# Optimization experiments

Hardware: AMD Instinct MI355X
Metric: run time of the kernel (lower is better)

Reference implementation:

```python
import jax, jax.numpy as jnp
import numpy as np

NUM_Q_HEADS = 16
NUM_KV_HEADS = 4
HEAD_DIM = 128
HIDDEN = NUM_Q_HEADS * HEAD_DIM
SCALE = 1.0 / HEAD_DIM ** 0.5
NUM_REP = NUM_Q_HEADS // NUM_KV_HEADS
S, B = 2048, 2


def setup_inputs() -> dict:
    key = jax.random.key(0)
    kq, kk, kv = jax.random.split(key, 3)
    query = jax.random.normal(kq, (S, B, NUM_Q_HEADS, HEAD_DIM), dtype=jnp.float32)
    k = jax.random.normal(kk, (S, B, NUM_KV_HEADS, HEAD_DIM), dtype=jnp.float32)
    v = jax.random.normal(kv, (S, B, NUM_KV_HEADS, HEAD_DIM), dtype=jnp.float32)
    return {"query": query, "key": k, "value": v}


def _attn(query, key, value):
    # GQA: repeat kv heads [S,B,Hkv,D] -> [S,B,Hq,D]
    key = jnp.repeat(key, NUM_REP, axis=2)
    value = jnp.repeat(value, NUM_REP, axis=2)
    # fp32 scores, causal mask, softmax (matches torch reference math)
    q32, k32, v32 = query.astype(jnp.float32), key.astype(jnp.float32), value.astype(jnp.float32)
    scores = jnp.einsum('sbhd,tbhd->bhst', q32, k32) * SCALE  # [B,Hq,S,S]
    s = scores.shape[-1]
    causal = jnp.tril(jnp.ones((s, s), dtype=bool))
    scores = jnp.where(causal, scores, -jnp.inf)
    attn = jax.nn.softmax(scores, axis=-1)
    out = jnp.einsum('bhst,tbhd->sbhd', attn, v32)  # [S,B,Hq,D]
    return out.astype(query.dtype).reshape(out.shape[0], out.shape[1], HIDDEN)


def reference(query, key, value) -> jnp.ndarray:
    return _attn(query, key, value)
```

## Files before the change

kernel.cpp:

```cpp
#include <hip/hip_runtime.h>
#include <cstdint>
#include <cstddef>

#define S_LEN 2048
#define BATCH 2
#define HQ    16
#define HKV   4
#define DH    128
#define KVB   64
#define QT0   64
#define KVB0  32
#define VP    40
#define PP    40

typedef float  f4     __attribute__((ext_vector_type(4)));
typedef float  f32x4  __attribute__((ext_vector_type(4)));
typedef float  f32x16 __attribute__((ext_vector_type(16)));
typedef short  short8 __attribute__((ext_vector_type(8)));
typedef unsigned u32x4 __attribute__((ext_vector_type(4)));
typedef __bf16 bf16x8 __attribute__((ext_vector_type(8)));

__device__ __forceinline__ unsigned short f2bf(float x) {
    unsigned u = __builtin_bit_cast(unsigned, x);
    u += 0x7fffu + ((u >> 16) & 1u);
    return (unsigned short)(u >> 16);
}
__device__ __forceinline__ void gld16(const void* g, void* l) {
    __builtin_amdgcn_global_load_lds(
        (const __attribute__((address_space(1))) unsigned int*)g,
        (__attribute__((address_space(3))) unsigned int*)l, 16, 0, 0);
}
__device__ __forceinline__ unsigned cvtpk_bf16(float lo, float hi) {
    unsigned r;
    asm("v_cvt_pk_bf16_f32 %0, %1, %2" : "=v"(r) : "v"(lo), "v"(hi));
    return r;
}

__global__ __launch_bounds__(256)
void prep_k(const float* __restrict__ K, short* __restrict__ out) {
    const int blk = blockIdx.x, bh = blk >> 5, tile = blk & 31, tid = threadIdx.x;
    const int r  = tid >> 2;
    const int s  = tile * 64 + r;
    const int c0 = (tid & 3) * 32;
    const float* src = K + ((size_t)s * (BATCH * HKV) + bh) * DH + c0;
    short* dst = out + ((size_t)bh * S_LEN + s) * DH;
    const int sw = (r & 7) << 3;
    #pragma unroll
    for (int ks = 0; ks < 4; ++ks) {
        f4 a  = ((const f4*)src)[ks * 2];
        f4 b2 = ((const f4*)src)[ks * 2 + 1];
        short8 o;
        #pragma unroll
        for (int j = 0; j < 4; ++j) { o[j] = (short)f2bf(a[j]); o[4 + j] = (short)f2bf(b2[j]); }
        *(short8*)&dst[(c0 + ks * 8) ^ sw] = o;
    }
}

__global__ __launch_bounds__(256)
void prep_v(const float* __restrict__ V, short* __restrict__ out) {
    __shared__ short t[64][136];
    const int blk = blockIdx.x, bh = blk >> 5, tile = blk & 31, tid = threadIdx.x;
    {
        const int r  = tid >> 2;
        const int c0 = (tid & 3) * 32;
        const float* src = V + ((size_t)(tile * 64 + r) * (BATCH * HKV) + bh) * DH + c0;
        #pragma unroll
        for (int m = 0; m < 8; ++m) {
            f4 x = ((const f4*)src)[m];
            #pragma unroll
            for (int j = 0; j < 4; ++j) t[r][c0 + m * 4 + j] = (short)f2bf(x[j]);
        }
    }
    __syncthreads();
    {
        const int d   = tid >> 1;
        const int cc0 = (tid & 1) * 32;
        const int sw  = (d & 7) << 3;
        short* dst = out + (size_t)bh * (S_LEN * DH) + (size_t)tile * (64 * DH) + d * 64 + cc0;
        #pragma unroll
        for (int c8 = 0; c8 < 4; ++c8) {
            const int base = (cc0 + c8 * 8) ^ sw;
            short8 v;
            #pragma unroll
            for (int j = 0; j < 8; ++j) v[j] = t[base + j][d];
            ((short8*)dst)[c8] = v;
        }
    }
}

__global__ __launch_bounds__(512, 2)
void fattn_main(const float* __restrict__ Q, const short* __restrict__ Kb,
                const short* __restrict__ Vb, float* __restrict__ O)
{
    __shared__ short kbufs[2][KVB * DH];
    __shared__ short vbufs[2][DH * KVB];
    __shared__ float xbuf[8][32];

    const int bh  = blockIdx.y;
    const int b   = bh >> 4, h = bh & 15, hkv = h >> 2;
    const int bh2 = b * HKV + hkv;
    const int px  = blockIdx.x;
    const int tid = threadIdx.x;
    const int wid = tid >> 6;
    const int lane = tid & 63;
    const int lq  = lane & 31;
    const int hi  = lane >> 5;

    const int qx   = (wid < 4) ? (15 - px) : px;
    const int wq0  = qx * 128 + (wid & 3) * 32;
    const int tmask = wq0 >> 6;
    const int ntiles = 2 * (15 - px) + 2;

    const float QS = 0.127517244f;
    bf16x8 qf[8];
    {
        const float* qp = Q + ((size_t)(wq0 + lq) * BATCH + b) * (HQ * DH) + h * DH + 8 * hi;
        #pragma unroll
        for (int dstp = 0; dstp < 8; ++dstp) {
            f4 v0 = ((const f4*)(qp + dstp * 16))[0];
            f4 v1 = ((const f4*)(qp + dstp * 16))[1];
            short8 tq;
            #pragma unroll
            for (int j = 0; j < 4; ++j) {
                tq[j]     = (short)f2bf(v0[j] * QS);
                tq[4 + j] = (short)f2bf(v1[j] * QS);
            }
            qf[dstp] = __builtin_bit_cast(bf16x8, tq);
        }
    }

    f32x16 accO[4];
    #pragma unroll
    for (int dblk = 0; dblk < 4; ++dblk)
        #pragma unroll
        for (int r = 0; r < 16; ++r) accO[dblk][r] = 0.f;
    float m = -3.0e38f, dsum = 0.f;

    const char* ksrc = (const char*)(Kb + (size_t)bh2 * S_LEN * DH);
    const char* vsrc = (const char*)(Vb + (size_t)bh2 * S_LEN * DH);

    auto stage = [&](int t, int bufi) {
        const char* src = (wid < 4 ? ksrc : vsrc) + (size_t)t * 16384 + (size_t)(wid & 3) * 4096;
        char* dst = (char*)(wid < 4 ? &kbufs[bufi][0] : &vbufs[bufi][0]) + (wid & 3) * 4096;
        #pragma unroll
        for (int i = 0; i < 4; ++i) gld16(src + i * 1024 + lane * 16, dst + i * 1024);
    };

    stage(0, 0);
    __syncthreads();

    for (int t = 0; t < ntiles; ++t) {
        const int cur = t & 1;
        if (t + 1 < ntiles) stage(t + 1, cur ^ 1);
        if (t <= tmask) {
            const short* kc = kbufs[cur];
            const short* vc = vbufs[cur];

            f32x16 s0, s1;
            #pragma unroll
            for (int r = 0; r < 16; ++r) { s0[r] = 0.f; s1[r] = 0.f; }
            const int ksw = (lq & 7) << 3;
            const int kr0 = lq * DH, kr1 = (32 + lq) * DH;
            __builtin_amdgcn_s_setprio(1);
            #pragma unroll
            for (int dstp = 0; dstp < 8; ++dstp) {
                const int off = (dstp * 16 + 8 * hi) ^ ksw;
                short8 k0 = *(const short8*)&kc[kr0 + off];
                short8 k1 = *(const short8*)&kc[kr1 + off];
                s0 = __builtin_amdgcn_mfma_f32_32x32x16_bf16(
                    __builtin_bit_cast(bf16x8, k0), qf[dstp], s0, 0, 0, 0);
                s1 = __builtin_amdgcn_mfma_f32_32x32x16_bf16(
                    __builtin_bit_cast(bf16x8, k1), qf[dstp], s1, 0, 0, 0);
            }
            __builtin_amdgcn_s_setprio(0);

            if (t == tmask) {
                const int q = wq0 + lq;
                const int kvb = t * 64 + 4 * hi;
                #pragma unroll
                for (int r = 0; r < 16; ++r) {
                    const int crow = (r & 3) + 8 * (r >> 2);
                    if (kvb + crow > q)      s0[r] = -3.0e38f;
                    if (kvb + 32 + crow > q) s1[r] = -3.0e38f;
                }
            }

            float pm = fmaxf(s0[0], s1[0]);
            #pragma unroll
            for (int r = 1; r < 16; ++r) pm = fmaxf(pm, fmaxf(s0[r], s1[r]));
            pm = fmaxf(pm, __shfl_xor(pm, 32));

            if (!__all(pm <= m + 8.0f)) {
                const float mn = fmaxf(m, pm);
                const float al = __builtin_amdgcn_exp2f(m - mn);
                m = mn;
                if (lane < 32) xbuf[wid][lq] = al;
                #pragma unroll
                for (int g = 0; g < 4; ++g) {
                    f4 av = *(const f4*)&xbuf[wid][g * 8 + 4 * hi];
                    #pragma unroll
                    for (int i2 = 0; i2 < 4; ++i2) {
                        #pragma unroll
                        for (int dblk = 0; dblk < 4; ++dblk)
                            accO[dblk][g * 4 + i2] *= av[i2];
                    }
                }
                dsum *= al;
            }

            float rs = 0.f;
            #pragma unroll
            for (int r = 0; r < 16; ++r) { s0[r] = __builtin_amdgcn_exp2f(s0[r] - m); rs += s0[r]; }
            #pragma unroll
            for (int r = 0; r < 16; ++r) { s1[r] = __builtin_amdgcn_exp2f(s1[r] - m); rs += s1[r]; }
            rs += __shfl_xor(rs, 32);
            dsum += rs;

            bf16x8 pf[4];
            #pragma unroll
            for (int kst = 0; kst < 4; ++kst) {
                const int bo = (kst & 1) * 8;
                float p0, p1, p2, p3, p4, p5, p6, p7;
                if (kst < 2) {
                    p0 = s0[bo + 0]; p1 = s0[bo + 1]; p2 = s0[bo + 2]; p3 = s0[bo + 3];
                    p4 = s0[bo + 4]; p5 = s0[bo + 5]; p6 = s0[bo + 6]; p7 = s0[bo + 7];
                } else {
                    p0 = s1[bo + 0]; p1 = s1[bo + 1]; p2 = s1[bo + 2]; p3 = s1[bo + 3];
                    p4 = s1[bo + 4]; p5 = s1[bo + 5]; p6 = s1[bo + 6]; p7 = s1[bo + 7];
                }
                const unsigned c0 = cvtpk_bf16(p0, p1);
                const unsigned c1 = cvtpk_bf16(p2, p3);
                const unsigned c2 = cvtpk_bf16(p4, p5);
                const unsigned c3 = cvtpk_bf16(p6, p7);
                const unsigned sc0 = (unsigned)__shfl_xor((int)c0, 32);
                const unsigned sc1 = (unsigned)__shfl_xor((int)c1, 32);
                const unsigned sc2 = (unsigned)__shfl_xor((int)c2, 32);
                const unsigned sc3 = (unsigned)__shfl_xor((int)c3, 32);
                u32x4 pw;
                pw[0] = hi ? sc2 : c0;
                pw[1] = hi ? sc3 : c1;
                pw[2] = hi ? c2  : sc0;
                pw[3] = hi ? c3  : sc1;
                pf[kst] = __builtin_bit_cast(bf16x8, pw);
            }

            const int vsw = (lq & 7) << 3;
            __builtin_amdgcn_s_setprio(1);
            #pragma unroll
            for (int kst = 0; kst < 4; ++kst) {
                const int voff = kst * 16 + 8 * hi;
                #pragma unroll
                for (int dblk = 0; dblk < 4; ++dblk) {
                    const int d = dblk * 32 + lq;
                    short8 vv = *(const short8*)&vc[d * KVB + ((voff) ^ vsw)];
                    accO[dblk] = __builtin_amdgcn_mfma_f32_32x32x16_bf16(
                        pf[kst], __builtin_bit_cast(bf16x8, vv), accO[dblk], 0, 0, 0);
                }
            }
            __builtin_amdgcn_s_setprio(0);
        }
        __syncthreads();
    }

    if (lane < 32) xbuf[wid][lq] = dsum;
    #pragma unroll
    for (int g = 0; g < 4; ++g) {
        f4 dv = *(const f4*)&xbuf[wid][g * 8 + 4 * hi];
        #pragma unroll
        for (int i2 = 0; i2 < 4; ++i2) {
            const float inv = 1.0f / dv[i2];
            const int row = wq0 + g * 8 + i2 + 4 * hi;
            float* op = O + ((size_t)row * BATCH + b) * (HQ * DH) + h * DH + lq;
            #pragma unroll
            for (int dblk = 0; dblk < 4; ++dblk)
                op[dblk * 32] = accO[dblk][g * 4 + i2] * inv;
        }
    }
}

__global__ __launch_bounds__(256)
void fattn_fallback(const float* __restrict__ Q, const float* __restrict__ K,
                    const float* __restrict__ V, float* __restrict__ O)
{
    __shared__ short kbuf[KVB0 * DH];
    __shared__ short vbuf[DH * VP];
    __shared__ short pbuf[4][16 * PP];

    const int bh  = blockIdx.y;
    const int b   = bh >> 4, h = bh & 15, hkv = h >> 2;
    const int q0  = blockIdx.x * QT0;
    const int tid = threadIdx.x;
    const int wid = tid >> 6;
    const int lane = tid & 63;
    const int lr  = lane & 15;
    const int kb  = lane >> 4;
    const int qr  = q0 + wid * 16;

    const float QS = 0.127517244f;
    bf16x8 qf[4];
    {
        const float* qp = Q + ((size_t)(qr + lr) * BATCH + b) * (HQ * DH) + h * DH + kb * 8;
        #pragma unroll
        for (int ks = 0; ks < 4; ++ks) {
            f4 v0 = ((const f4*)(qp + ks * 32))[0];
            f4 v1 = ((const f4*)(qp + ks * 32))[1];
            short8 tq;
            #pragma unroll
            for (int j = 0; j < 4; ++j) {
                tq[j]     = (short)f2bf(v0[j] * QS);
                tq[4 + j] = (short)f2bf(v1[j] * QS);
            }
            qf[ks] = __builtin_bit_cast(bf16x8, tq);
        }
    }

    float mr[4], ls[4];
    f32x4 accO[8];
    #pragma unroll
    for (int r = 0; r < 4; ++r) { mr[r] = -3.0e38f; ls[r] = 0.0f; }
    #pragma unroll
    for (int d = 0; d < 8; ++d) accO[d] = (f32x4){0.f, 0.f, 0.f, 0.f};

    const int sr  = tid >> 3, sc = tid & 7;
    const int vr2 = (tid >> 4) * 2, vc8 = tid & 15;
    const int ntiles = q0 / KVB0 + 2;

    for (int t = 0; t < ntiles; ++t) {
        const int kv0 = t * KVB0;
        {
            const float* kp = K + ((size_t)(kv0 + sr) * BATCH + b) * (HKV * DH) + hkv * DH + sc * 16;
            f4 a0 = ((const f4*)kp)[0];
            f4 a1 = ((const f4*)kp)[1];
            f4 a2 = ((const f4*)kp)[2];
            f4 a3 = ((const f4*)kp)[3];
            short8 s0v, s1v;
            #pragma unroll
            for (int j = 0; j < 4; ++j) {
                s0v[j] = (short)f2bf(a0[j]); s0v[4 + j] = (short)f2bf(a1[j]);
                s1v[j] = (short)f2bf(a2[j]); s1v[4 + j] = (short)f2bf(a3[j]);
            }
            const int sw = (sr & 7) << 3;
            *(short8*)&kbuf[sr * DH + ((sc * 16) ^ sw)]     = s0v;
            *(short8*)&kbuf[sr * DH + ((sc * 16 + 8) ^ sw)] = s1v;
        }
        {
            const float* vp0 = V + ((size_t)(kv0 + vr2) * BATCH + b) * (HKV * DH) + hkv * DH + vc8 * 8;
            const float* vp1 = vp0 + (size_t)BATCH * HKV * DH;
            f4 b0 = ((const f4*)vp0)[0];
            f4 b1 = ((const f4*)vp0)[1];
            f4 c0 = ((const f4*)vp1)[0];
            f4 c1 = ((const f4*)vp1)[1];
            float va[8]  = {b0[0], b0[1], b0[2], b0[3], b1[0], b1[1], b1[2], b1[3]};
            float vbv[8] = {c0[0], c0[1], c0[2], c0[3], c1[0], c1[1], c1[2], c1[3]};
            #pragma unroll
            for (int j = 0; j < 8; ++j) {
                const int d = vc8 * 8 + j;
                unsigned pk = (unsigned)f2bf(va[j]) | ((unsigned)f2bf(vbv[j]) << 16);
                const int rsw = (((vr2 >> 3) ^ ((d >> 3) & 3)) << 3) + (vr2 & 7);
                *(unsigned*)&vbuf[d * VP + rsw] = pk;
            }
        }
        __syncthreads();

        f32x4 sf[2];
        sf[0] = (f32x4){0.f, 0.f, 0.f, 0.f};
        sf[1] = (f32x4){0.f, 0.f, 0.f, 0.f};
        #pragma unroll
        for (int cb = 0; cb < 2; ++cb) {
            const int krow = cb * 16 + lr;
            const int sw = (krow & 7) << 3;
            #pragma unroll
            for (int ks = 0; ks < 4; ++ks) {
                short8 kkf = *(const short8*)&kbuf[krow * DH + ((ks * 32 + kb * 8) ^ sw)];
                sf[cb] = __builtin_amdgcn_mfma_f32_16x16x32_bf16(
                    qf[ks], __builtin_bit_cast(bf16x8, kkf), sf[cb], 0, 0, 0);
            }
        }
        if (kv0 + KVB0 - 1 > qr) {
            #pragma unroll
            for (int cb = 0; cb < 2; ++cb) {
                const int col = kv0 + cb * 16 + lr;
                #pragma unroll
                for (int r = 0; r < 4; ++r)
                    if (col > qr + kb * 4 + r) sf[cb][r] = -3.0e38f;
            }
        }
        float al[4];
        #pragma unroll
        for (int r = 0; r < 4; ++r) {
            float rm = fmaxf(sf[0][r], sf[1][r]);
            rm = fmaxf(rm, __shfl_xor(rm, 1));
            rm = fmaxf(rm, __shfl_xor(rm, 2));
            rm = fmaxf(rm, __shfl_xor(rm, 4));
            rm = fmaxf(rm, __shfl_xor(rm, 8));
            const float mn = fmaxf(mr[r], rm);
            al[r] = exp2f(mr[r] - mn);
            mr[r] = mn;
            const unsigned short pk0 = f2bf(exp2f(sf[0][r] - mn));
            const unsigned short pk1 = f2bf(exp2f(sf[1][r] - mn));
            pbuf[wid][(kb * 4 + r) * PP + lr]      = (short)pk0;
            pbuf[wid][(kb * 4 + r) * PP + 16 + lr] = (short)pk1;
            float ps = __builtin_bit_cast(float, (unsigned)pk0 << 16)
                     + __builtin_bit_cast(float, (unsigned)pk1 << 16);
            ps += __shfl_xor(ps, 1);
            ps += __shfl_xor(ps, 2);
            ps += __shfl_xor(ps, 4);
            ps += __shfl_xor(ps, 8);
            ls[r] = ls[r] * al[r] + ps;
        }
        #pragma unroll
        for (int d = 0; d < 8; ++d) {
            #pragma unroll
            for (int r = 0; r < 4; ++r) accO[d][r] *= al[r];
        }
        const short8 pA = *(const short8*)&pbuf[wid][lr * PP + kb * 8];
        #pragma unroll
        for (int db = 0; db < 8; ++db) {
            const int d = db * 16 + lr;
            const int rc = ((kb ^ ((d >> 3) & 3)) << 3);
            short8 vv = *(const short8*)&vbuf[d * VP + rc];
            accO[db] = __builtin_amdgcn_mfma_f32_16x16x32_bf16(
                __builtin_bit_cast(bf16x8, pA), __builtin_bit_cast(bf16x8, vv), accO[db], 0, 0, 0);
        }
        __syncthreads();
    }

    #pragma unroll
    for (int r = 0; r < 4; ++r) ls[r] = 1.0f / ls[r];
    #pragma unroll
    for (int db = 0; db < 8; ++db) {
        #pragma unroll
        for (int r = 0; r < 4; ++r) {
            const int row = qr + kb * 4 + r;
            O[((size_t)row * BATCH + b) * (HQ * DH) + h * DH + db * 16 + lr] = accO[db][r] * ls[r];
        }
    }
}

extern "C" void kernel_launch(void* const* d_in, const int* in_sizes, int n_in,
                              void* d_out, int out_size, void* d_ws, size_t ws_size,
                              hipStream_t stream)
{
    (void)in_sizes; (void)n_in; (void)out_size;
    const float* Q = (const float*)d_in[0];
    const float* K = (const float*)d_in[1];
    const float* V = (const float*)d_in[2];
    float* O = (float*)d_out;

    const size_t kv_elems = (size_t)BATCH * HKV * S_LEN * DH;
    const size_t need = kv_elems * 2 * sizeof(short);
    if (ws_size >= need) {
        short* Kb = (short*)d_ws;
        short* Vb = Kb + kv_elems;
        prep_k<<<dim3(BATCH * HKV * (S_LEN / 64)), dim3(256), 0, stream>>>(K, Kb);
        prep_v<<<dim3(BATCH * HKV * (S_LEN / 64)), dim3(256), 0, stream>>>(V, Vb);
        dim3 grid(8, BATCH * HQ);
        fattn_main<<<grid, dim3(512), 0, stream>>>(Q, Kb, Vb, O);
    } else {
        dim3 grid(S_LEN / QT0, BATCH * HQ);
        fattn_fallback<<<grid, dim3(256), 0, stream>>>(Q, K, V, O);
    }
}
```

Measured before the change: 81.12 us.

## Split KV range across two warp halves per query block and merge partials

```diff
diff --git a/kernel.cpp b/kernel.cpp
--- a/kernel.cpp
+++ b/kernel.cpp
@@ -88,28 +88,26 @@
     }
 }
 
-__global__ __launch_bounds__(512, 2)
+__global__ __launch_bounds__(512, 1)
 void fattn_main(const float* __restrict__ Q, const short* __restrict__ Kb,
                 const short* __restrict__ Vb, float* __restrict__ O)
 {
-    __shared__ short kbufs[2][KVB * DH];
-    __shared__ short vbufs[2][DH * KVB];
+    __shared__ short kb[2][2][KVB * DH];
+    __shared__ short vb[2][2][DH * KVB];
     __shared__ float xbuf[8][32];
 
-    const int bh  = blockIdx.y;
+    const int bh  = blockIdx.x;
     const int b   = bh >> 4, h = bh & 15, hkv = h >> 2;
     const int bh2 = b * HKV + hkv;
-    const int px  = blockIdx.x;
+    const int qx  = 15 - (int)blockIdx.y;
     const int tid = threadIdx.x;
     const int wid = tid >> 6;
     const int lane = tid & 63;
     const int lq  = lane & 31;
     const int hi  = lane >> 5;
-
-    const int qx   = (wid < 4) ? (15 - px) : px;
+    const int half = wid >> 2;
     const int wq0  = qx * 128 + (wid & 3) * 32;
-    const int tmask = wq0 >> 6;
-    const int ntiles = 2 * (15 - px) + 2;
+    const int nlo  = qx + 1;
 
     const float QS = 0.127517244f;
     bf16x8 qf[8];
@@ -139,22 +137,26 @@
     const char* ksrc = (const char*)(Kb + (size_t)bh2 * S_LEN * DH);
     const char* vsrc = (const char*)(Vb + (size_t)bh2 * S_LEN * DH);
 
-    auto stage = [&](int t, int bufi) {
-        const char* src = (wid < 4 ? ksrc : vsrc) + (size_t)t * 16384 + (size_t)(wid & 3) * 4096;
-        char* dst = (char*)(wid < 4 ? &kbufs[bufi][0] : &vbufs[bufi][0]) + (wid & 3) * 4096;
-        #pragma unroll
-        for (int i = 0; i < 4; ++i) gld16(src + i * 1024 + lane * 16, dst + i * 1024);
+    auto stage = [&](int i) {
+        const int tile = (wid >> 2) ? (nlo + i) : i;
+        const int isV  = (wid >> 1) & 1;
+        const char* src = (isV ? vsrc : ksrc) + (size_t)tile * 16384 + (size_t)(wid & 1) * 8192;
+        char* dst = (isV ? (char*)&vb[wid >> 2][i & 1][0] : (char*)&kb[wid >> 2][i & 1][0])
+                    + (wid & 1) * 8192;
+        #pragma unroll
+        for (int j = 0; j < 8; ++j) gld16(src + j * 1024 + lane * 16, dst + j * 1024);
     };
 
-    stage(0, 0);
-    __syncthreads();
-
-    for (int t = 0; t < ntiles; ++t) {
-        const int cur = t & 1;
-        if (t + 1 < ntiles) stage(t + 1, cur ^ 1);
-        if (t <= tmask) {
-            const short* kc = kbufs[cur];
-            const short* vc = vbufs[cur];
+    stage(0);
+    __syncthreads();
+
+    for (int i = 0; i < nlo; ++i) {
+        if (i + 1 < nlo) stage(i + 1);
+        const int t   = half ? (nlo + i) : i;
+        const int kv0 = t * 64;
+        if (kv0 <= wq0 + 31) {
+            const short* kc = kb[half][i & 1];
+            const short* vc = vb[half][i & 1];
 
             f32x16 s0, s1;
             #pragma unroll
@@ -174,9 +176,9 @@
             }
             __builtin_amdgcn_s_setprio(0);
 
-            if (t == tmask) {
+            if (kv0 + 63 > wq0) {
                 const int q = wq0 + lq;
-                const int kvb = t * 64 + 4 * hi;
+                const int kvb = kv0 + 4 * hi;
                 #pragma unroll
                 for (int r = 0; r < 16; ++r) {
                     const int crow = (r & 3) + 8 * (r >> 2);
@@ -252,7 +254,7 @@
                 #pragma unroll
                 for (int dblk = 0; dblk < 4; ++dblk) {
                     const int d = dblk * 32 + lq;
-                    short8 vv = *(const short8*)&vc[d * KVB + ((voff) ^ vsw)];
+                    short8 vv = *(const short8*)&vc[d * KVB + (voff ^ vsw)];
                     accO[dblk] = __builtin_amdgcn_mfma_f32_32x32x16_bf16(
                         pf[kst], __builtin_bit_cast(bf16x8, vv), accO[dblk], 0, 0, 0);
                 }
@@ -262,18 +264,66 @@
         __syncthreads();
     }
 
+    if (lane < 32) xbuf[wid][lq] = m;
+    __syncthreads();
+    const float mo = xbuf[wid ^ 4][lq];
+    const float ms = fmaxf(m, mo);
+    const float aa = __builtin_amdgcn_exp2f(m - ms);
+    dsum *= aa;
+    __syncthreads();
     if (lane < 32) xbuf[wid][lq] = dsum;
+    __syncthreads();
+    dsum += xbuf[wid ^ 4][lq];
+    __syncthreads();
+    if (lane < 32) xbuf[wid][lq] = aa;
     #pragma unroll
     for (int g = 0; g < 4; ++g) {
-        f4 dv = *(const f4*)&xbuf[wid][g * 8 + 4 * hi];
+        f4 av = *(const f4*)&xbuf[wid][g * 8 + 4 * hi];
         #pragma unroll
         for (int i2 = 0; i2 < 4; ++i2) {
-            const float inv = 1.0f / dv[i2];
-            const int row = wq0 + g * 8 + i2 + 4 * hi;
-            float* op = O + ((size_t)row * BATCH + b) * (HQ * DH) + h * DH + lq;
             #pragma unroll
             for (int dblk = 0; dblk < 4; ++dblk)
-                op[dblk * 32] = accO[dblk][g * 4 + i2] * inv;
+                accO[dblk][g * 4 + i2] *= av[i2];
+        }
+    }
+    __syncthreads();
+    float* mb = (float*)&kb[0][0][0];
+    if (half) {
+        float* slot = mb + (size_t)(wid & 3) * 4096;
+        #pragma unroll
+        for (int dblk = 0; dblk < 4; ++dblk)
+            #pragma unroll
+            for (int r2 = 0; r2 < 4; ++r2) {
+                f4 v;
+                #pragma unroll
+                for (int j = 0; j < 4; ++j) v[j] = accO[dblk][r2 * 4 + j];
+                *(f4*)&slot[(dblk * 4 + r2) * 256 + lane * 4] = v;
+            }
+    }
+    __syncthreads();
+    if (!half) {
+        float* slot = mb + (size_t)(wid & 3) * 4096;
+        #pragma unroll
+        for (int dblk = 0; dblk < 4; ++dblk)
+            #pragma unroll
+            for (int r2 = 0; r2 < 4; ++r2) {
+                f4 v = *(const f4*)&slot[(dblk * 4 + r2) * 256 + lane * 4];
+                #pragma unroll
+                for (int j = 0; j < 4; ++j) accO[dblk][r2 * 4 + j] += v[j];
+            }
+        if (lane < 32) xbuf[wid][lq] = dsum;
+        #pragma unroll
+        for (int g = 0; g < 4; ++g) {
+            f4 dv = *(const f4*)&xbuf[wid][g * 8 + 4 * hi];
+            #pragma unroll
+            for (int i2 = 0; i2 < 4; ++i2) {
+                const float inv = 1.0f / dv[i2];
+                const int row = wq0 + g * 8 + i2 + 4 * hi;
+                float* op = O + ((size_t)row * BATCH + b) * (HQ * DH) + h * DH + lq;
+                #pragma unroll
+                for (int dblk = 0; dblk < 4; ++dblk)
+                    op[dblk * 32] = accO[dblk][g * 4 + i2] * inv;
+            }
         }
     }
 }
@@ -293,13 +343,13 @@
     const int wid = tid >> 6;
     const int lane = tid & 63;
     const int lr  = lane & 15;
-    const int kb  = lane >> 4;
+    const int kb2 = lane >> 4;
     const int qr  = q0 + wid * 16;
 
     const float QS = 0.127517244f;
     bf16x8 qf[4];
     {
-        const float* qp = Q + ((size_t)(qr + lr) * BATCH + b) * (HQ * DH) + h * DH + kb * 8;
+        const float* qp = Q + ((size_t)(qr + lr) * BATCH + b) * (HQ * DH) + h * DH + kb2 * 8;
         #pragma unroll
         for (int ks = 0; ks < 4; ++ks) {
             f4 v0 = ((const f4*)(qp + ks * 32))[0];
@@ -371,7 +421,7 @@
             const int sw = (krow & 7) << 3;
             #pragma unroll
             for (int ks = 0; ks < 4; ++ks) {
-                short8 kkf = *(const short8*)&kbuf[krow * DH + ((ks * 32 + kb * 8) ^ sw)];
+                short8 kkf = *(const short8*)&kbuf[krow * DH + ((ks * 32 + kb2 * 8) ^ sw)];
                 sf[cb] = __builtin_amdgcn_mfma_f32_16x16x32_bf16(
                     qf[ks], __builtin_bit_cast(bf16x8, kkf), sf[cb], 0, 0, 0);
             }
@@ -382,7 +432,7 @@
                 const int col = kv0 + cb * 16 + lr;
                 #pragma unroll
                 for (int r = 0; r < 4; ++r)
-                    if (col > qr + kb * 4 + r) sf[cb][r] = -3.0e38f;
+                    if (col > qr + kb2 * 4 + r) sf[cb][r] = -3.0e38f;
             }
         }
         float al[4];
@@ -398,8 +448,8 @@
             mr[r] = mn;
             const unsigned short pk0 = f2bf(exp2f(sf[0][r] - mn));
             const unsigned short pk1 = f2bf(exp2f(sf[1][r] - mn));
-            pbuf[wid][(kb * 4 + r) * PP + lr]      = (short)pk0;
-            pbuf[wid][(kb * 4 + r) * PP + 16 + lr] = (short)pk1;
+            pbuf[wid][(kb2 * 4 + r) * PP + lr]      = (short)pk0;
+            pbuf[wid][(kb2 * 4 + r) * PP + 16 + lr] = (short)pk1;
             float ps = __builtin_bit_cast(float, (unsigned)pk0 << 16)
                      + __builtin_bit_cast(float, (unsigned)pk1 << 16);
             ps += __shfl_xor(ps, 1);
@@ -413,11 +463,11 @@
             #pragma unroll
             for (int r = 0; r < 4; ++r) accO[d][r] *= al[r];
         }
-        const short8 pA = *(const short8*)&pbuf[wid][lr * PP + kb * 8];
+        const short8 pA = *(const short8*)&pbuf[wid][lr * PP + kb2 * 8];
         #pragma unroll
         for (int db = 0; db < 8; ++db) {
             const int d = db * 16 + lr;
-            const int rc = ((kb ^ ((d >> 3) & 3)) << 3);
+            const int rc = ((kb2 ^ ((d >> 3) & 3)) << 3);
             short8 vv = *(const short8*)&vbuf[d * VP + rc];
             accO[db] = __builtin_amdgcn_mfma_f32_16x16x32_bf16(
                 __builtin_bit_cast(bf16x8, pA), __builtin_bit_cast(bf16x8, vv), accO[db], 0, 0, 0);
@@ -431,7 +481,7 @@
     for (int db = 0; db < 8; ++db) {
         #pragma unroll
         for (int r = 0; r < 4; ++r) {
-            const int row = qr + kb * 4 + r;
+            const int row = qr + kb2 * 4 + r;
             O[((size_t)row * BATCH + b) * (HQ * DH) + h * DH + db * 16 + lr] = accO[db][r] * ls[r];
         }
     }
@@ -454,7 +504,7 @@
         short* Vb = Kb + kv_elems;
         prep_k<<<dim3(BATCH * HKV * (S_LEN / 64)), dim3(256), 0, stream>>>(K, Kb);
         prep_v<<<dim3(BATCH * HKV * (S_LEN / 64)), dim3(256), 0, stream>>>(V, Vb);
-        dim3 grid(8, BATCH * HQ);
+        dim3 grid(BATCH * HQ, 16);
         fattn_main<<<grid, dim3(512), 0, stream>>>(Q, Kb, Vb, O);
     } else {
         dim3 grid(S_LEN / QT0, BATCH * HQ);
```

After: 74.88 us. 1.08x faster.

## Split head dimension across warp halves and give each block one query tile

Applied to the files above, without the earlier changes.

```diff
diff --git a/kernel.cpp b/kernel.cpp
--- a/kernel.cpp
+++ b/kernel.cpp
@@ -92,24 +92,23 @@
 void fattn_main(const float* __restrict__ Q, const short* __restrict__ Kb,
                 const short* __restrict__ Vb, float* __restrict__ O)
 {
-    __shared__ short kbufs[2][KVB * DH];
-    __shared__ short vbufs[2][DH * KVB];
+    __shared__ short kv[2][2][8192];
     __shared__ float xbuf[8][32];
 
-    const int bh  = blockIdx.y;
+    const int bh  = blockIdx.x;
     const int b   = bh >> 4, h = bh & 15, hkv = h >> 2;
     const int bh2 = b * HKV + hkv;
-    const int px  = blockIdx.x;
+    const int y   = blockIdx.y;
+    const int qx  = (y < 8) ? (15 - y) : (y - 8);
     const int tid = threadIdx.x;
     const int wid = tid >> 6;
     const int lane = tid & 63;
     const int lq  = lane & 31;
     const int hi  = lane >> 5;
-
-    const int qx   = (wid < 4) ? (15 - px) : px;
-    const int wq0  = qx * 128 + (wid & 3) * 32;
-    const int tmask = wq0 >> 6;
-    const int ntiles = 2 * (15 - px) + 2;
+    const int rw  = wid & 3;
+    const int dh  = wid >> 2;
+    const int wq0 = qx * 128 + rw * 32;
+    const int ntiles = 2 * qx + 2;
 
     const float QS = 0.127517244f;
     bf16x8 qf[8];
@@ -129,9 +128,9 @@
         }
     }
 
-    f32x16 accO[4];
-    #pragma unroll
-    for (int dblk = 0; dblk < 4; ++dblk)
+    f32x16 accO[2];
+    #pragma unroll
+    for (int dblk = 0; dblk < 2; ++dblk)
         #pragma unroll
         for (int r = 0; r < 16; ++r) accO[dblk][r] = 0.f;
     float m = -3.0e38f, dsum = 0.f;
@@ -141,9 +140,9 @@
 
     auto stage = [&](int t, int bufi) {
         const char* src = (wid < 4 ? ksrc : vsrc) + (size_t)t * 16384 + (size_t)(wid & 3) * 4096;
-        char* dst = (char*)(wid < 4 ? &kbufs[bufi][0] : &vbufs[bufi][0]) + (wid & 3) * 4096;
-        #pragma unroll
-        for (int i = 0; i < 4; ++i) gld16(src + i * 1024 + lane * 16, dst + i * 1024);
+        char* dst = (char*)&kv[bufi][wid >= 4 ? 1 : 0][0] + (wid & 3) * 4096;
+        #pragma unroll
+        for (int j = 0; j < 4; ++j) gld16(src + j * 1024 + lane * 16, dst + j * 1024);
     };
 
     stage(0, 0);
@@ -152,9 +151,10 @@
     for (int t = 0; t < ntiles; ++t) {
         const int cur = t & 1;
         if (t + 1 < ntiles) stage(t + 1, cur ^ 1);
-        if (t <= tmask) {
-            const short* kc = kbufs[cur];
-            const short* vc = vbufs[cur];
+        const int kv0 = t * 64;
+        if (kv0 <= wq0 + 31) {
+            const short* kc = &kv[cur][0][0];
+            const short* vc = &kv[cur][1][0];
 
             f32x16 s0, s1;
             #pragma unroll
@@ -174,9 +174,9 @@
             }
             __builtin_amdgcn_s_setprio(0);
 
-            if (t == tmask) {
+            if (kv0 + 63 > wq0) {
                 const int q = wq0 + lq;
-                const int kvb = t * 64 + 4 * hi;
+                const int kvb = kv0 + 4 * hi;
                 #pragma unroll
                 for (int r = 0; r < 16; ++r) {
                     const int crow = (r & 3) + 8 * (r >> 2);
@@ -201,7 +201,7 @@
                     #pragma unroll
                     for (int i2 = 0; i2 < 4; ++i2) {
                         #pragma unroll
-                        for (int dblk = 0; dblk < 4; ++dblk)
+                        for (int dblk = 0; dblk < 2; ++dblk)
                             accO[dblk][g * 4 + i2] *= av[i2];
                     }
                 }
@@ -250,9 +250,9 @@
             for (int kst = 0; kst < 4; ++kst) {
                 const int voff = kst * 16 + 8 * hi;
                 #pragma unroll
-                for (int dblk = 0; dblk < 4; ++dblk) {
-                    const int d = dblk * 32 + lq;
-                    short8 vv = *(const short8*)&vc[d * KVB + ((voff) ^ vsw)];
+                for (int dblk = 0; dblk < 2; ++dblk) {
+                    const int d = dh * 64 + dblk * 32 + lq;
+                    short8 vv = *(const short8*)&vc[d * KVB + (voff ^ vsw)];
                     accO[dblk] = __builtin_amdgcn_mfma_f32_32x32x16_bf16(
                         pf[kst], __builtin_bit_cast(bf16x8, vv), accO[dblk], 0, 0, 0);
                 }
@@ -270,9 +270,9 @@
         for (int i2 = 0; i2 < 4; ++i2) {
             const float inv = 1.0f / dv[i2];
             const int row = wq0 + g * 8 + i2 + 4 * hi;
-            float* op = O + ((size_t)row * BATCH + b) * (HQ * DH) + h * DH + lq;
-            #pragma unroll
-            for (int dblk = 0; dblk < 4; ++dblk)
+            float* op = O + ((size_t)row * BATCH + b) * (HQ * DH) + h * DH + dh * 64 + lq;
+            #pragma unroll
+            for (int dblk = 0; dblk < 2; ++dblk)
                 op[dblk * 32] = accO[dblk][g * 4 + i2] * inv;
         }
     }
@@ -293,13 +293,13 @@
     const int wid = tid >> 6;
     const int lane = tid & 63;
     const int lr  = lane & 15;
-    const int kb  = lane >> 4;
+    const int kb2 = lane >> 4;
     const int qr  = q0 + wid * 16;
 
     const float QS = 0.127517244f;
     bf16x8 qf[4];
     {
-        const float* qp = Q + ((size_t)(qr + lr) * BATCH + b) * (HQ * DH) + h * DH + kb * 8;
+        const float* qp = Q + ((size_t)(qr + lr) * BATCH + b) * (HQ * DH) + h * DH + kb2 * 8;
         #pragma unroll
         for (int ks = 0; ks < 4; ++ks) {
             f4 v0 = ((const f4*)(qp + ks * 32))[0];
@@ -371,7 +371,7 @@
             const int sw = (krow & 7) << 3;
             #pragma unroll
             for (int ks = 0; ks < 4; ++ks) {
-                short8 kkf = *(const short8*)&kbuf[krow * DH + ((ks * 32 + kb * 8) ^ sw)];
+                short8 kkf = *(const short8*)&kbuf[krow * DH + ((ks * 32 + kb2 * 8) ^ sw)];
                 sf[cb] = __builtin_amdgcn_mfma_f32_16x16x32_bf16(
                     qf[ks], __builtin_bit_cast(bf16x8, kkf), sf[cb], 0, 0, 0);
             }
@@ -382,7 +382,7 @@
                 const int col = kv0 + cb * 16 + lr;
                 #pragma unroll
                 for (int r = 0; r < 4; ++r)
-                    if (col > qr + kb * 4 + r) sf[cb][r] = -3.0e38f;
+                    if (col > qr + kb2 * 4 + r) sf[cb][r] = -3.0e38f;
             }
         }
         float al[4];
@@ -398,8 +398,8 @@
             mr[r] = mn;
             const unsigned short pk0 = f2bf(exp2f(sf[0][r] - mn));
             const unsigned short pk1 = f2bf(exp2f(sf[1][r] - mn));
-            pbuf[wid][(kb * 4 + r) * PP + lr]      = (short)pk0;
-            pbuf[wid][(kb * 4 + r) * PP + 16 + lr] = (short)pk1;
+            pbuf[wid][(kb2 * 4 + r) * PP + lr]      = (short)pk0;
+            pbuf[wid][(kb2 * 4 + r) * PP + 16 + lr] = (short)pk1;
             float ps = __builtin_bit_cast(float, (unsigned)pk0 << 16)
                      + __builtin_bit_cast(float, (unsigned)pk1 << 16);
             ps += __shfl_xor(ps, 1);
@@ -413,11 +413,11 @@
             #pragma unroll
             for (int r = 0; r < 4; ++r) accO[d][r] *= al[r];
         }
-        const short8 pA = *(const short8*)&pbuf[wid][lr * PP + kb * 8];
+        const short8 pA = *(const short8*)&pbuf[wid][lr * PP + kb2 * 8];
         #pragma unroll
         for (int db = 0; db < 8; ++db) {
             const int d = db * 16 + lr;
-            const int rc = ((kb ^ ((d >> 3) & 3)) << 3);
+            const int rc = ((kb2 ^ ((d >> 3) & 3)) << 3);
             short8 vv = *(const short8*)&vbuf[d * VP + rc];
             accO[db] = __builtin_amdgcn_mfma_f32_16x16x32_bf16(
                 __builtin_bit_cast(bf16x8, pA), __builtin_bit_cast(bf16x8, vv), accO[db], 0, 0, 0);
@@ -431,7 +431,7 @@
     for (int db = 0; db < 8; ++db) {
         #pragma unroll
         for (int r = 0; r < 4; ++r) {
-            const int row = qr + kb * 4 + r;
+            const int row = qr + kb2 * 4 + r;
             O[((size_t)row * BATCH + b) * (HQ * DH) + h * DH + db * 16 + lr] = accO[db][r] * ls[r];
         }
     }
@@ -454,7 +454,7 @@
         short* Vb = Kb + kv_elems;
         prep_k<<<dim3(BATCH * HKV * (S_LEN / 64)), dim3(256), 0, stream>>>(K, Kb);
         prep_v<<<dim3(BATCH * HKV * (S_LEN / 64)), dim3(256), 0, stream>>>(V, Vb);
-        dim3 grid(8, BATCH * HQ);
+        dim3 grid(BATCH * HQ, 16);
         fattn_main<<<grid, dim3(512), 0, stream>>>(Q, Kb, Vb, O);
     } else {
         dim3 grid(S_LEN / QT0, BATCH * HQ);
```

New measurement: 119.3 us. +47.0%, slower.
